# Kernel optimization log

Hardware: AMD Instinct MI355X
Metric: run time of the kernel (lower is better)

The kernel has to match this reference:

```python
import jax, jax.numpy as jnp
import numpy as np
from jax.scipy.special import xlogy

W_BI = 0.5
W_TRI = 0.5
EPS = 1e-10


def setup_inputs() -> dict:
    key = jax.random.key(0)
    B, L, V = 8, 2048, 512
    logits = jax.random.normal(key, (B, L, V), dtype=jnp.float32)
    return {"logits": logits}


def _safe_normalized_entropy(joint, max_log):
    # 1 - H(joint)/H_max (concentration penalty), fp32-safe
    joint = joint / (joint.sum() + EPS)
    entropy = -xlogy(joint, jnp.clip(joint, EPS, None)).sum()
    return jnp.clip(1.0 - entropy / (max_log + EPS), 0.0, 1.0)


def reference(logits):
    x = jnp.nan_to_num(logits.astype(jnp.float32), nan=0.0, posinf=80.0, neginf=-80.0)
    p = jax.nn.softmax(x, axis=-1)  # (B, L, V)
    B, L, V = p.shape
    max_log_bi = float(np.log(float(V * V)))
    max_log_tri = float(np.log(float(V) ** 3))

    total = jnp.zeros((), dtype=jnp.float32)

    # Bigram joint distribution over (V, V)
    bigram_joint = jnp.einsum('nla,nlb->ab', p[:, :-1, :], p[:, 1:, :])
    total = total + W_BI * _safe_normalized_entropy(bigram_joint, max_log_bi)

    # Trigram: (V,V) bigram part outer-producted with third-position marginal -> (V,V,V)
    bi_part = jnp.einsum('nla,nlb->ab', p[:, :-2, :], p[:, 1:-1, :])
    tri_joint = jnp.einsum('ab,nlc->abc', bi_part, p[:, 2:, :])
    total = total + W_TRI * _safe_normalized_entropy(tri_joint, max_log_tri)

    return jnp.clip(jnp.nan_to_num(total, nan=0.0, posinf=1.0), 0.0, 1.0)
```

## Files before the change

kernel.cpp:

```cpp
#include <hip/hip_runtime.h>
#include <math.h>

#define L_SEQ 2048
#define V 512
#define NROWS 16384
#define LDT 16448
#define NSPLIT 16
#define EPS 1e-10

typedef __bf16 bf16x8 __attribute__((ext_vector_type(8)));
typedef float f32x4 __attribute__((ext_vector_type(4)));

#define PT_OFF  ((size_t)0)
#define GP_OFF  ((size_t)512 * LDT * 2)
#define RB_OFF  (GP_OFF + (size_t)NSPLIT * V * V * 4)
#define M_OFF   (RB_OFF + (size_t)23 * V * 4)
#define PC_OFF  (M_OFF + (size_t)V * 4)
#define MP_OFF  (PC_OFF + (size_t)1024 * 4 * 8)

#define GLDS16(g, l) __builtin_amdgcn_global_load_lds( \
    (const __attribute__((address_space(1))) unsigned int*)(g), \
    (__attribute__((address_space(3))) unsigned int*)(l), 16, 0, 0)

__device__ __forceinline__ unsigned short f2bf(float f) {
    unsigned u = __float_as_uint(f);
    unsigned r = (u + 0x7fffu + ((u >> 16) & 1u)) >> 16;
    return (unsigned short)r;
}

__device__ __forceinline__ void softmax_row_bf16(const float* __restrict__ x,
                                                 int lane, unsigned short* out) {
    float4 va = *(const float4*)(x + lane * 4);
    float4 vb = *(const float4*)(x + 256 + lane * 4);
    float v[8] = {va.x, va.y, va.z, va.w, vb.x, vb.y, vb.z, vb.w};
    float e[8];
    float s = 0.0f;
#pragma unroll
    for (int i = 0; i < 8; i++) {
        float xi = fminf(fmaxf(v[i], -80.0f), 80.0f);
        e[i] = __expf(xi);
        s += e[i];
    }
#pragma unroll
    for (int o = 32; o; o >>= 1) s += __shfl_xor(s, o, 64);
    float inv = 1.0f / s;
#pragma unroll
    for (int i = 0; i < 8; i++) out[i] = f2bf(e[i] * inv);
}

__global__ __launch_bounds__(256) void softmaxT_k(const float* __restrict__ in,
                                                  unsigned short* __restrict__ pT,
                                                  float* __restrict__ rb,
                                                  float* __restrict__ mp) {
    __shared__ __align__(16) unsigned short sm[32 * 512];
    int t = threadIdx.x;
    int w = t >> 6, lane = t & 63;
    if (blockIdx.x >= 512) {
        int j = blockIdx.x - 512;
        if (w == 0) {
            int r = j < 8 ? j * L_SEQ + L_SEQ - 2
                  : j < 16 ? (j - 8) * L_SEQ + L_SEQ - 1
                  : (j - 15) * L_SEQ;
            unsigned short o[8];
            softmax_row_bf16(in + (size_t)r * V, lane, o);
#pragma unroll
            for (int i = 0; i < 4; i++)
                rb[j * V + lane * 4 + i] = __uint_as_float((unsigned)o[i] << 16);
#pragma unroll
            for (int i = 0; i < 4; i++)
                rb[j * V + 256 + lane * 4 + i] = __uint_as_float((unsigned)o[4 + i] << 16);
        }
        return;
    }
    int k0 = blockIdx.x * 32;
#pragma unroll
    for (int i = 0; i < 8; i++) {
        int rr = w * 8 + i;
        unsigned short o[8];
        softmax_row_bf16(in + (size_t)(k0 + rr) * V, lane, o);
        *(ushort4*)&sm[rr * 512 + lane * 4] = make_ushort4(o[0], o[1], o[2], o[3]);
        *(ushort4*)&sm[rr * 512 + 256 + lane * 4] = make_ushort4(o[4], o[5], o[6], o[7]);
    }
    __syncthreads();
    int cA = 2 * t, cB = cA + 1;
    unsigned u[32];
#pragma unroll
    for (int k = 0; k < 32; k++) u[k] = *(const unsigned*)&sm[k * 512 + cA];
    bool excl = ((blockIdx.x & 63) == 0);
    float mA = 0.0f, mB = 0.0f;
#pragma unroll
    for (int k = 0; k < 32; k++) {
        if (excl && k < 2) continue;
        mA += __uint_as_float(u[k] << 16);
        mB += __uint_as_float(u[k] & 0xffff0000u);
    }
    *(float2*)&mp[(size_t)blockIdx.x * 512 + cA] = make_float2(mA, mB);
    unsigned oA[16], oB[16];
#pragma unroll
    for (int i = 0; i < 16; i++) {
        unsigned e0 = u[2 * i], e1 = u[2 * i + 1];
        oA[i] = (e0 & 0xffffu) | (e1 << 16);
        oB[i] = (e0 >> 16) | (e1 & 0xffff0000u);
    }
    uint4* dA = (uint4*)(pT + (size_t)cA * LDT + k0);
    uint4* dB = (uint4*)(pT + (size_t)cB * LDT + k0);
#pragma unroll
    for (int i = 0; i < 4; i++) {
        dA[i] = make_uint4(oA[4 * i], oA[4 * i + 1], oA[4 * i + 2], oA[4 * i + 3]);
        dB[i] = make_uint4(oB[4 * i], oB[4 * i + 1], oB[4 * i + 2], oB[4 * i + 3]);
    }
    if (blockIdx.x == 511) {
#pragma unroll
        for (int j = 0; j < 8; j++) {
            *(uint4*)(pT + (size_t)cA * LDT + 16384 + 8 * j) = make_uint4(0, 0, 0, 0);
            *(uint4*)(pT + (size_t)cB * LDT + 16384 + 8 * j) = make_uint4(0, 0, 0, 0);
        }
    }
}

__global__ __launch_bounds__(256) void gemm_k(const unsigned short* __restrict__ pT,
                                              float* __restrict__ gp) {
    __shared__ __align__(16) uint4 ldsA[512];
    __shared__ __align__(16) uint4 ldsB[256];
    int b = blockIdx.x;
    int xcd = b & 7, j = b >> 3;
    int split = xcd * 2 + (j >> 5);
    int tile = j & 31;
    int ta = (tile >> 3) * 128, tb = (tile & 7) * 64;
    int t = threadIdx.x, w = t >> 6, lane = t & 63;
    int l15 = lane & 15, q = lane >> 4;
    int wa = (w & 1) * 64, wb = (w >> 1) * 32;
    int k0base = split * 1024;

    f32x4 acc[4][2];
#pragma unroll
    for (int g = 0; g < 4; g++)
#pragma unroll
        for (int h = 0; h < 2; h++) acc[g][h] = (f32x4){0.f, 0.f, 0.f, 0.f};

    int srowA = 16 * w + (lane >> 2);
    int qoffA = (lane & 3) * 8;
    const size_t rA1 = (size_t)(ta + srowA) * LDT;
    const size_t rA2 = (size_t)(ta + 64 + srowA) * LDT;
    int qoffB = (t & 3) * 8;
    const size_t rB = (size_t)(tb + (t >> 2)) * LDT;

    for (int it = 0; it < 32; it++) {
        int kelA = k0base + it * 32 + qoffA;
        int kelB = k0base + it * 32 + qoffB;
        const unsigned short* gb = pT + rB + kelB;
        uint4 x1 = *(const uint4*)gb;
        unsigned y1 = *(const unsigned*)(gb + 8);
        __syncthreads();
        GLDS16(pT + rA1 + kelA, &ldsA[64 * w]);
        GLDS16(pT + rA2 + kelA, &ldsA[256 + 64 * w]);
        uint4 s1;
        s1.x = (x1.x >> 16) | (x1.y << 16);
        s1.y = (x1.y >> 16) | (x1.z << 16);
        s1.z = (x1.z >> 16) | (x1.w << 16);
        s1.w = (x1.w >> 16) | (y1 << 16);
        ldsB[t] = s1;
        __syncthreads();
        bf16x8 af[4], bv[2];
#pragma unroll
        for (int g = 0; g < 4; g++)
            af[g] = __builtin_bit_cast(bf16x8, ldsA[4 * (wa + g * 16 + l15) + q]);
#pragma unroll
        for (int h = 0; h < 2; h++)
            bv[h] = __builtin_bit_cast(bf16x8, ldsB[4 * (wb + h * 16 + l15) + q]);
#pragma unroll
        for (int g = 0; g < 4; g++)
#pragma unroll
            for (int h = 0; h < 2; h++)
                acc[g][h] = __builtin_amdgcn_mfma_f32_16x16x32_bf16(af[g], bv[h], acc[g][h], 0, 0, 0);
    }

    float* og = gp + (size_t)split * V * V;
#pragma unroll
    for (int g = 0; g < 4; g++) {
        int a = ta + wa + g * 16 + q * 4;
#pragma unroll
        for (int h = 0; h < 2; h++) {
            int b2 = tb + wb + h * 16 + l15;
#pragma unroll
            for (int r = 0; r < 4; r++)
                og[(size_t)(a + r) * V + b2] = acc[g][h][r];
        }
    }
}

__global__ __launch_bounds__(256) void reduce_k(const float* __restrict__ mp,
                                                const float* __restrict__ gp,
                                                const float* __restrict__ rb,
                                                float* __restrict__ m,
                                                double* __restrict__ pc) {
    int bid = blockIdx.x, t = threadIdx.x;
    if (bid < 16) {
        int c = bid * 32 + (t & 31);
        int seg = t >> 5;
        float s = 0.0f;
#pragma unroll
        for (int i = 0; i < 64; i++)
            s += mp[(size_t)(seg * 64 + i) * 512 + c];
        __shared__ float redm[8][32];
        redm[seg][t & 31] = s;
        __syncthreads();
        if (t < 32) {
            float acc = 0.0f;
#pragma unroll
            for (int sgi = 0; sgi < 8; sgi++) acc += redm[sgi][t];
            m[bid * 32 + t] = acc;
        }
    } else {
        int idx = (bid - 16) * 256 + t;
        int a = idx >> 9, b = idx & (V - 1);
        double ga = 0, gb2 = 0, gc = 0, gd = 0;
#pragma unroll
        for (int s = 0; s < NSPLIT; s += 4) {
            ga += (double)gp[(size_t)(s + 0) * V * V + idx];
            gb2 += (double)gp[(size_t)(s + 1) * V * V + idx];
            gc += (double)gp[(size_t)(s + 2) * V * V + idx];
            gd += (double)gp[(size_t)(s + 3) * V * V + idx];
        }
        double g = (ga + gb2) + (gc + gd);
        float cross = 0.f, cc = 0.f;
#pragma unroll
        for (int n = 0; n < 7; n++)
            cross = fmaf(rb[(8 + n) * V + a], rb[(16 + n) * V + b], cross);
#pragma unroll
        for (int n = 0; n < 8; n++)
            cc = fmaf(rb[n * V + a], rb[(8 + n) * V + b], cc);
        double g1 = g - (double)cross;
        double g2 = g1 - (double)cc;
        double s1 = g1, t1 = g1 * (double)logf((float)g1);
        double s2 = g2, t2 = g2 * (double)logf((float)g2);
#pragma unroll
        for (int o = 32; o; o >>= 1) {
            s1 += __shfl_xor(s1, o, 64);
            t1 += __shfl_xor(t1, o, 64);
            s2 += __shfl_xor(s2, o, 64);
            t2 += __shfl_xor(t2, o, 64);
        }
        __shared__ double redg[4][4];
        if ((t & 63) == 0) {
            int w = t >> 6;
            redg[w][0] = s1; redg[w][1] = t1; redg[w][2] = s2; redg[w][3] = t2;
        }
        __syncthreads();
        if (t == 0) {
            double* o = pc + (size_t)(bid - 16) * 4;
            o[0] = redg[0][0] + redg[1][0] + redg[2][0] + redg[3][0];
            o[1] = redg[0][1] + redg[1][1] + redg[2][1] + redg[3][1];
            o[2] = redg[0][2] + redg[1][2] + redg[2][2] + redg[3][2];
            o[3] = redg[0][3] + redg[1][3] + redg[2][3] + redg[3][3];
        }
    }
}

__global__ __launch_bounds__(512) void final_k(const float* __restrict__ m,
                                               const double* __restrict__ pc,
                                               float* __restrict__ out) {
    int t = threadIdx.x;
    double s1 = 0, t1 = 0, s2 = 0, t2 = 0;
#pragma unroll
    for (int j = 0; j < 2; j++) {
        const double* q = pc + (size_t)(t + 512 * j) * 4;
        s1 += q[0]; t1 += q[1]; s2 += q[2]; t2 += q[3];
    }
    double mv = (double)m[t];
    double sm = mv;
    double tm = mv * log(mv);
#pragma unroll
    for (int o = 32; o; o >>= 1) {
        sm += __shfl_xor(sm, o, 64);
        tm += __shfl_xor(tm, o, 64);
        s1 += __shfl_xor(s1, o, 64);
        t1 += __shfl_xor(t1, o, 64);
        s2 += __shfl_xor(s2, o, 64);
        t2 += __shfl_xor(t2, o, 64);
    }
    __shared__ double red[6][8];
    if ((t & 63) == 0) {
        int w = t >> 6;
        red[0][w] = sm; red[1][w] = tm;
        red[2][w] = s1; red[3][w] = t1;
        red[4][w] = s2; red[5][w] = t2;
    }
    __syncthreads();
    if (t == 0) {
        double acc[6];
        for (int i = 0; i < 6; i++) {
            acc[i] = 0;
            for (int w = 0; w < 8; w++) acc[i] += red[i][w];
        }
        double Sm = acc[0], Tm = acc[1];
        double S1 = acc[2], T1 = acc[3], S2 = acc[4], T2 = acc[5];
        double D1 = S1 + EPS;
        double Hbi = (log(D1) * S1 - T1) / D1;
        double mlb = log((double)V * (double)V);
        double cbi = 1.0 - Hbi / (mlb + EPS);
        cbi = fmin(fmax(cbi, 0.0), 1.0);
        double S3 = S2 * Sm;
        double D3 = S3 + EPS;
        double Htri = (log(D3) * S3 - (Sm * T2 + S2 * Tm)) / D3;
        double mlt = log((double)V * (double)V * (double)V);
        double ctri = 1.0 - Htri / (mlt + EPS);
        ctri = fmin(fmax(ctri, 0.0), 1.0);
        double tot = 0.5 * cbi + 0.5 * ctri;
        if (!(tot == tot)) tot = 0.0;
        tot = fmin(fmax(tot, 0.0), 1.0);
        out[0] = (float)tot;
    }
}

extern "C" void kernel_launch(void* const* d_in, const int* in_sizes, int n_in,
                              void* d_out, int out_size, void* d_ws, size_t ws_size,
                              hipStream_t stream) {
    (void)in_sizes; (void)n_in; (void)out_size; (void)ws_size;
    const float* logits = (const float*)d_in[0];
    float* out = (float*)d_out;
    char* ws = (char*)d_ws;
    unsigned short* pT = (unsigned short*)(ws + PT_OFF);
    float* gp = (float*)(ws + GP_OFF);
    float* rb = (float*)(ws + RB_OFF);
    float* m = (float*)(ws + M_OFF);
    double* pc = (double*)(ws + PC_OFF);
    float* mp = (float*)(ws + MP_OFF);

    softmaxT_k<<<535, 256, 0, stream>>>(logits, pT, rb, mp);
    gemm_k<<<512, 256, 0, stream>>>(pT, gp);
    reduce_k<<<1040, 256, 0, stream>>>(mp, gp, rb, m, pc);
    final_k<<<1, 512, 0, stream>>>(m, pc, out);
}
```

Before: 113.7 us.

## Double-buffer GEMM LDS tiles and fold final reduction into last reduce block

The GEMM main loop now uses two LDS buffers, so the next K-slice is prefetched (global_load_lds for A, register load and shift for B) while MFMAs run on the current slice, with one barrier per iteration instead of two. The separate single-block final kernel is removed. The last reduce block to finish, detected with an atomic counter that the GEMM kernel resets, now computes the final entropy combination. This saves a kernel launch and hides load latency, at the cost of twice the LDS and reliance on threadfence and atomic ordering for correctness.

```diff
diff --git a/kernel.cpp b/kernel.cpp
--- a/kernel.cpp
+++ b/kernel.cpp
@@ -17,6 +17,7 @@
 #define M_OFF   (RB_OFF + (size_t)23 * V * 4)
 #define PC_OFF  (M_OFF + (size_t)V * 4)
 #define MP_OFF  (PC_OFF + (size_t)1024 * 4 * 8)
+#define CTR_OFF (MP_OFF + (size_t)V * V * 4)
 
 #define GLDS16(g, l) __builtin_amdgcn_global_load_lds( \
     (const __attribute__((address_space(1))) unsigned int*)(g), \
@@ -119,9 +120,11 @@
 }
 
 __global__ __launch_bounds__(256) void gemm_k(const unsigned short* __restrict__ pT,
-                                              float* __restrict__ gp) {
-    __shared__ __align__(16) uint4 ldsA[512];
-    __shared__ __align__(16) uint4 ldsB[256];
+                                              float* __restrict__ gp,
+                                              unsigned* __restrict__ ctr) {
+    __shared__ __align__(16) uint4 ldsA[2][512];
+    __shared__ __align__(16) uint4 ldsB[2][256];
+    if (blockIdx.x == 0 && threadIdx.x == 0) *ctr = 0u;
     int b = blockIdx.x;
     int xcd = b & 7, j = b >> 3;
     int split = xcd * 2 + (j >> 5);
@@ -145,34 +148,57 @@
     int qoffB = (t & 3) * 8;
     const size_t rB = (size_t)(tb + (t >> 2)) * LDT;
 
-    for (int it = 0; it < 32; it++) {
-        int kelA = k0base + it * 32 + qoffA;
-        int kelB = k0base + it * 32 + qoffB;
+    {
+        int kelA = k0base + qoffA;
+        int kelB = k0base + qoffB;
+        GLDS16(pT + rA1 + kelA, &ldsA[0][64 * w]);
+        GLDS16(pT + rA2 + kelA, &ldsA[0][256 + 64 * w]);
         const unsigned short* gb = pT + rB + kelB;
         uint4 x1 = *(const uint4*)gb;
         unsigned y1 = *(const unsigned*)(gb + 8);
-        __syncthreads();
-        GLDS16(pT + rA1 + kelA, &ldsA[64 * w]);
-        GLDS16(pT + rA2 + kelA, &ldsA[256 + 64 * w]);
         uint4 s1;
         s1.x = (x1.x >> 16) | (x1.y << 16);
         s1.y = (x1.y >> 16) | (x1.z << 16);
         s1.z = (x1.z >> 16) | (x1.w << 16);
         s1.w = (x1.w >> 16) | (y1 << 16);
-        ldsB[t] = s1;
+        ldsB[0][t] = s1;
         __syncthreads();
+    }
+
+    for (int it = 0; it < 32; it++) {
+        int cur = it & 1, nxt = cur ^ 1;
+        uint4 x1;
+        unsigned y1;
+        if (it < 31) {
+            int kelA = k0base + (it + 1) * 32 + qoffA;
+            int kelB = k0base + (it + 1) * 32 + qoffB;
+            GLDS16(pT + rA1 + kelA, &ldsA[nxt][64 * w]);
+            GLDS16(pT + rA2 + kelA, &ldsA[nxt][256 + 64 * w]);
+            const unsigned short* gb = pT + rB + kelB;
+            x1 = *(const uint4*)gb;
+            y1 = *(const unsigned*)(gb + 8);
+        }
         bf16x8 af[4], bv[2];
 #pragma unroll
         for (int g = 0; g < 4; g++)
-            af[g] = __builtin_bit_cast(bf16x8, ldsA[4 * (wa + g * 16 + l15) + q]);
+            af[g] = __builtin_bit_cast(bf16x8, ldsA[cur][4 * (wa + g * 16 + l15) + q]);
 #pragma unroll
         for (int h = 0; h < 2; h++)
-            bv[h] = __builtin_bit_cast(bf16x8, ldsB[4 * (wb + h * 16 + l15) + q]);
+            bv[h] = __builtin_bit_cast(bf16x8, ldsB[cur][4 * (wb + h * 16 + l15) + q]);
 #pragma unroll
         for (int g = 0; g < 4; g++)
 #pragma unroll
             for (int h = 0; h < 2; h++)
                 acc[g][h] = __builtin_amdgcn_mfma_f32_16x16x32_bf16(af[g], bv[h], acc[g][h], 0, 0, 0);
+        if (it < 31) {
+            uint4 s1;
+            s1.x = (x1.x >> 16) | (x1.y << 16);
+            s1.y = (x1.y >> 16) | (x1.z << 16);
+            s1.z = (x1.z >> 16) | (x1.w << 16);
+            s1.w = (x1.w >> 16) | (y1 << 16);
+            ldsB[nxt][t] = s1;
+        }
+        __syncthreads();
     }
 
     float* og = gp + (size_t)split * V * V;
@@ -193,7 +219,9 @@
                                                 const float* __restrict__ gp,
                                                 const float* __restrict__ rb,
                                                 float* __restrict__ m,
-                                                double* __restrict__ pc) {
+                                                double* __restrict__ pc,
+                                                unsigned* __restrict__ ctr,
+                                                float* __restrict__ out) {
     int bid = blockIdx.x, t = threadIdx.x;
     if (bid < 16) {
         int c = bid * 32 + (t & 31);
@@ -255,21 +283,28 @@
             o[3] = redg[0][3] + redg[1][3] + redg[2][3] + redg[3][3];
         }
     }
-}
-
-__global__ __launch_bounds__(512) void final_k(const float* __restrict__ m,
-                                               const double* __restrict__ pc,
-                                               float* __restrict__ out) {
-    int t = threadIdx.x;
+
+    __syncthreads();
+    __threadfence();
+    __shared__ unsigned done;
+    if (t == 0) done = atomicAdd(ctr, 1u);
+    __syncthreads();
+    if (done != 1039u) return;
+    __threadfence();
+
     double s1 = 0, t1 = 0, s2 = 0, t2 = 0;
 #pragma unroll
+    for (int j = 0; j < 4; j++) {
+        const double* qd = pc + (size_t)(t + 256 * j) * 4;
+        s1 += qd[0]; t1 += qd[1]; s2 += qd[2]; t2 += qd[3];
+    }
+    double sm = 0, tm = 0;
+#pragma unroll
     for (int j = 0; j < 2; j++) {
-        const double* q = pc + (size_t)(t + 512 * j) * 4;
-        s1 += q[0]; t1 += q[1]; s2 += q[2]; t2 += q[3];
-    }
-    double mv = (double)m[t];
-    double sm = mv;
-    double tm = mv * log(mv);
+        double mv = (double)m[t + 256 * j];
+        sm += mv;
+        tm += mv * log(mv);
+    }
 #pragma unroll
     for (int o = 32; o; o >>= 1) {
         sm += __shfl_xor(sm, o, 64);
@@ -279,7 +314,7 @@
         s2 += __shfl_xor(s2, o, 64);
         t2 += __shfl_xor(t2, o, 64);
     }
-    __shared__ double red[6][8];
+    __shared__ double red[6][4];
     if ((t & 63) == 0) {
         int w = t >> 6;
         red[0][w] = sm; red[1][w] = tm;
@@ -291,7 +326,7 @@
         double acc[6];
         for (int i = 0; i < 6; i++) {
             acc[i] = 0;
-            for (int w = 0; w < 8; w++) acc[i] += red[i][w];
+            for (int w = 0; w < 4; w++) acc[i] += red[i][w];
         }
         double Sm = acc[0], Tm = acc[1];
         double S1 = acc[2], T1 = acc[3], S2 = acc[4], T2 = acc[5];
@@ -326,9 +361,9 @@
     float* m = (float*)(ws + M_OFF);
     double* pc = (double*)(ws + PC_OFF);
     float* mp = (float*)(ws + MP_OFF);
+    unsigned* ctr = (unsigned*)(ws + CTR_OFF);
 
     softmaxT_k<<<535, 256, 0, stream>>>(logits, pT, rb, mp);
-    gemm_k<<<512, 256, 0, stream>>>(pT, gp);
-    reduce_k<<<1040, 256, 0, stream>>>(mp, gp, rb, m, pc);
-    final_k<<<1, 512, 0, stream>>>(m, pc, out);
-}
+    gemm_k<<<512, 256, 0, stream>>>(pT, gp, ctr);
+    reduce_k<<<1040, 256, 0, stream>>>(mp, gp, rb, m, pc, ctr, out);
+}
```

Result: slower. 173.4 us (+52.6%).

## Double-buffer LDS tiles in bigram GEMM to overlap loads with MFMA

Applied to the files above, without the earlier changes.

The GEMM kernel now keeps two LDS buffers for the A and B tiles. While the current k-slice is multiplied with MFMA, the next slice is prefetched: A via global_load_lds and B via register loads that are shifted and written to LDS after the MFMAs. This cuts one barrier per iteration and hides global load latency behind compute, at the cost of twice the LDS per block and more live registers.

```diff
diff --git a/kernel.cpp b/kernel.cpp
--- a/kernel.cpp
+++ b/kernel.cpp
@@ -120,8 +120,8 @@
 
 __global__ __launch_bounds__(256) void gemm_k(const unsigned short* __restrict__ pT,
                                               float* __restrict__ gp) {
-    __shared__ __align__(16) uint4 ldsA[512];
-    __shared__ __align__(16) uint4 ldsB[256];
+    __shared__ __align__(16) uint4 ldsA[2][512];
+    __shared__ __align__(16) uint4 ldsB[2][256];
     int b = blockIdx.x;
     int xcd = b & 7, j = b >> 3;
     int split = xcd * 2 + (j >> 5);
@@ -145,34 +145,57 @@
     int qoffB = (t & 3) * 8;
     const size_t rB = (size_t)(tb + (t >> 2)) * LDT;
 
-    for (int it = 0; it < 32; it++) {
-        int kelA = k0base + it * 32 + qoffA;
-        int kelB = k0base + it * 32 + qoffB;
+    {
+        int kelA = k0base + qoffA;
+        int kelB = k0base + qoffB;
+        GLDS16(pT + rA1 + kelA, &ldsA[0][64 * w]);
+        GLDS16(pT + rA2 + kelA, &ldsA[0][256 + 64 * w]);
         const unsigned short* gb = pT + rB + kelB;
         uint4 x1 = *(const uint4*)gb;
         unsigned y1 = *(const unsigned*)(gb + 8);
-        __syncthreads();
-        GLDS16(pT + rA1 + kelA, &ldsA[64 * w]);
-        GLDS16(pT + rA2 + kelA, &ldsA[256 + 64 * w]);
         uint4 s1;
         s1.x = (x1.x >> 16) | (x1.y << 16);
         s1.y = (x1.y >> 16) | (x1.z << 16);
         s1.z = (x1.z >> 16) | (x1.w << 16);
         s1.w = (x1.w >> 16) | (y1 << 16);
-        ldsB[t] = s1;
+        ldsB[0][t] = s1;
         __syncthreads();
+    }
+
+    for (int it = 0; it < 32; it++) {
+        int cur = it & 1, nxt = cur ^ 1;
+        uint4 x1;
+        unsigned y1;
+        if (it < 31) {
+            int kelA = k0base + (it + 1) * 32 + qoffA;
+            int kelB = k0base + (it + 1) * 32 + qoffB;
+            GLDS16(pT + rA1 + kelA, &ldsA[nxt][64 * w]);
+            GLDS16(pT + rA2 + kelA, &ldsA[nxt][256 + 64 * w]);
+            const unsigned short* gb = pT + rB + kelB;
+            x1 = *(const uint4*)gb;
+            y1 = *(const unsigned*)(gb + 8);
+        }
         bf16x8 af[4], bv[2];
 #pragma unroll
         for (int g = 0; g < 4; g++)
-            af[g] = __builtin_bit_cast(bf16x8, ldsA[4 * (wa + g * 16 + l15) + q]);
+            af[g] = __builtin_bit_cast(bf16x8, ldsA[cur][4 * (wa + g * 16 + l15) + q]);
 #pragma unroll
         for (int h = 0; h < 2; h++)
-            bv[h] = __builtin_bit_cast(bf16x8, ldsB[4 * (wb + h * 16 + l15) + q]);
+            bv[h] = __builtin_bit_cast(bf16x8, ldsB[cur][4 * (wb + h * 16 + l15) + q]);
 #pragma unroll
         for (int g = 0; g < 4; g++)
 #pragma unroll
             for (int h = 0; h < 2; h++)
                 acc[g][h] = __builtin_amdgcn_mfma_f32_16x16x32_bf16(af[g], bv[h], acc[g][h], 0, 0, 0);
+        if (it < 31) {
+            uint4 s1;
+            s1.x = (x1.x >> 16) | (x1.y << 16);
+            s1.y = (x1.y >> 16) | (x1.z << 16);
+            s1.z = (x1.z >> 16) | (x1.w << 16);
+            s1.w = (x1.w >> 16) | (y1 << 16);
+            ldsB[nxt][t] = s1;
+        }
+        __syncthreads();
     }
 
     float* og = gp + (size_t)split * V * V;
```

Result: no change. 114.9 us (+1.1%).
